# Kernel optimization log

Measured on AMD Instinct MI355X. Metric: run time of the kernel, lower is better.

## Reference

```python
import jax, jax.numpy as jnp
import numpy as np

NUM_GROUPS = 32
EPS = 1e-6


def group_norm(x, gamma, beta):
    # x: [B, C, H, W]; GroupNorm over (channels-in-group, H, W)
    B, C, H, W = x.shape
    xg = x.reshape(B, NUM_GROUPS, C // NUM_GROUPS, H, W)
    mean = xg.mean(axis=(2, 3, 4), keepdims=True)
    var = xg.var(axis=(2, 3, 4), keepdims=True)
    xn = ((xg - mean) * jax.lax.rsqrt(var + EPS)).reshape(B, C, H, W)
    return xn * gamma[None, :, None, None] + beta[None, :, None, None]


def conv1x1(x, w, b):
    # 1x1 conv == channel-mixing matmul. w: [C_out, C_in]
    return jnp.einsum('bchw,oc->bohw', x, w) + b[None, :, None, None]


def setup_inputs() -> dict:
    key = jax.random.key(0)
    ks = jax.random.split(key, 6)
    B, C, H, W = 8, 256, 64, 64
    s = 1.0 / np.sqrt(C)  # fan-in scaled weights (like Conv2d default)
    inp = {
        'x': jax.random.normal(ks[0], (B, C, H, W), jnp.float32),
        'gamma': jnp.ones((C,), jnp.float32),
        'beta': jnp.zeros((C,), jnp.float32),
        'wq': jax.random.normal(ks[1], (C, C), jnp.float32) * s,
        'bq': jnp.zeros((C,), jnp.float32),
        'wk': jax.random.normal(ks[2], (C, C), jnp.float32) * s,
        'bk': jnp.zeros((C,), jnp.float32),
        'wv': jax.random.normal(ks[3], (C, C), jnp.float32) * s,
        'bv': jnp.zeros((C,), jnp.float32),
        'wo': jax.random.normal(ks[4], (C, C), jnp.float32) * s,
        'bo': jnp.zeros((C,), jnp.float32),
    }
    return inp


def reference(x, gamma, beta, wq, bq, wk, bk, wv, bv, wo, bo):
    B, C, H, W = x.shape
    h = group_norm(x, gamma, beta)
    q = conv1x1(h, wq, bq)
    k = conv1x1(h, wk, bk)
    v = conv1x1(h, wv, bv)
    # elu + 1 feature map (nonnegative kernel features)
    q = jax.nn.elu(q) + 1.0
    k = jax.nn.elu(k) + 1.0
    N = H * W
    kf = k.reshape(B, C, N)            # [B, C, N]
    vf = v.reshape(B, C, N)            # [B, C, N]
    qf = q.reshape(B, C, N)            # [B, C, N]
    # kv = k @ v^T : [B, C, C]
    kv = jnp.einsum('bcn,bdn->bcd', kf, vf)
    # h_out[b, n, d] = sum_c q[b, c, n] * kv[b, c, d]; stored channel-first
    h_out = jnp.einsum('bcn,bcd->bdn', qf, kv).reshape(B, C, H, W)
    return x + conv1x1(h_out, wo, bo)
```

## Files before the change

### kernel.cpp

```cpp
#include <hip/hip_runtime.h>
#include <math.h>

#define C_DIM 256
#define N_DIM 4096
#define B_DIM 8

typedef __attribute__((ext_vector_type(8))) short bf16x8;
typedef __attribute__((ext_vector_type(4))) float f32x4;
typedef __attribute__((ext_vector_type(8))) unsigned short us8;
typedef __attribute__((ext_vector_type(4))) unsigned short us4;

__device__ inline unsigned short f2bf(float f) {
    unsigned int u = __float_as_uint(f);
    u += 0x7fffu + ((u >> 16) & 1u);
    return (unsigned short)(u >> 16);
}

__device__ inline void gload_lds16(const void* g, void* l) {
    __builtin_amdgcn_global_load_lds(
        (const __attribute__((address_space(1))) unsigned int*)g,
        (__attribute__((address_space(3))) unsigned int*)l, 16, 0, 0);
}

__global__ __launch_bounds__(256) void prep_kernel(
    const float* __restrict__ wq, const float* __restrict__ wk,
    const float* __restrict__ wv, const float* __restrict__ wo,
    const float* __restrict__ bk, const float* __restrict__ bv,
    const float* __restrict__ x,
    unsigned short* __restrict__ wqb, unsigned short* __restrict__ wkvb,
    unsigned short* __restrict__ wob, float* __restrict__ bkv,
    float2* __restrict__ sums)
{
    int z = blockIdx.x;
    int t = threadIdx.x;
    if (z < 256) {
        const float* s; unsigned short* d;
        int which = z >> 6;
        if (which == 0)      { s = wq; d = wqb; }
        else if (which == 1) { s = wk; d = wkvb; }
        else if (which == 2) { s = wv; d = wkvb + 65536; }
        else                 { s = wo; d = wob; }
        int idx = (z & 63) * 1024 + t * 4;
        float4 v = *(const float4*)(s + idx);
        us4 r; r[0] = f2bf(v.x); r[1] = f2bf(v.y); r[2] = f2bf(v.z); r[3] = f2bf(v.w);
        *(us4*)(d + idx) = r;
    } else if (z == 256) {
        bkv[t]       = bk[t];
        bkv[t + 256] = bv[t];
    } else {
        int bc = z - 257;
        const float* xc = x + (size_t)bc * N_DIM;
        float s = 0.f, q = 0.f;
        for (int i = t; i < 1024; i += 256) {
            float4 v = ((const float4*)xc)[i];
            s += v.x + v.y + v.z + v.w;
            q += v.x*v.x + v.y*v.y + v.z*v.z + v.w*v.w;
        }
        #pragma unroll
        for (int off = 32; off > 0; off >>= 1) {
            s += __shfl_down(s, off);
            q += __shfl_down(q, off);
        }
        __shared__ float red[8];
        int w = t >> 6;
        if ((t & 63) == 0) { red[w*2] = s; red[w*2+1] = q; }
        __syncthreads();
        if (t == 0) {
            sums[bc] = make_float2(red[0]+red[2]+red[4]+red[6],
                                   red[1]+red[3]+red[5]+red[7]);
        }
    }
}

__global__ __launch_bounds__(256) void gn_apply(const float* __restrict__ x,
                                                const float2* __restrict__ sums,
                                                const float* __restrict__ gamma,
                                                const float* __restrict__ beta,
                                                unsigned short* __restrict__ hT) {
    int b = blockIdx.y, n0 = blockIdx.x * 64;
    int t = threadIdx.x;
    __shared__ float scale[256], shift[256];
    __shared__ unsigned short trans[64][264];

    {
        int c = t;
        int gbase = c & ~7;
        float s = 0.f, q = 0.f;
        #pragma unroll
        for (int j = 0; j < 8; j++) {
            float2 u = sums[b*256 + gbase + j];
            s += u.x; q += u.y;
        }
        float mean = s * (1.f/32768.f);
        float var  = q * (1.f/32768.f) - mean*mean;
        float inv  = rsqrtf(var + 1e-6f);
        float gm = gamma[c] * inv;
        scale[c] = gm;
        shift[c] = beta[c] - mean * gm;
    }
    __syncthreads();

    #pragma unroll
    for (int it = 0; it < 16; it++) {
        int c  = it*16 + (t >> 4);
        int nl = (t & 15) * 4;
        float4 v = *(const float4*)(x + ((size_t)(b*C_DIM + c))*N_DIM + n0 + nl);
        float sc = scale[c], sh = shift[c];
        trans[nl+0][c] = f2bf(v.x*sc + sh);
        trans[nl+1][c] = f2bf(v.y*sc + sh);
        trans[nl+2][c] = f2bf(v.z*sc + sh);
        trans[nl+3][c] = f2bf(v.w*sc + sh);
    }
    __syncthreads();

    #pragma unroll
    for (int it = 0; it < 8; it++) {
        int nl = it*8 + (t >> 5);
        int cb = (t & 31) * 8;
        us8 vv = *(us8*)&trans[nl][cb];
        *(us8*)(hT + ((size_t)b*N_DIM + n0 + nl)*C_DIM + cb) = vv;
    }
}

__global__ __launch_bounds__(256) void kvred(const float* __restrict__ src, unsigned short* __restrict__ dst) {
    int gi = (blockIdx.x * 256 + threadIdx.x) * 4;
    int b = gi >> 16, idx = gi & 65535;
    float4 a = make_float4(0.f,0.f,0.f,0.f);
    #pragma unroll
    for (int sp = 0; sp < 16; sp++) {
        float4 v = *(const float4*)(src + (((size_t)b*16 + sp) << 16) + idx);
        a.x += v.x; a.y += v.y; a.z += v.z; a.w += v.w;
    }
    us4 r; r[0] = f2bf(a.x); r[1] = f2bf(a.y); r[2] = f2bf(a.z); r[3] = f2bf(a.w);
    *(us4*)(dst + ((size_t)b << 16) + idx) = r;
}

template<int MODE>
__device__ __forceinline__ void gemm_body(
    const unsigned short* __restrict__ Ab, const unsigned short* __restrict__ Bb,
    const float* __restrict__ bias, const float* __restrict__ residb,
    void* __restrict__ Cb,
    int N, int K, int k0, int Ks, int m_blk, int n_blk, bool elu,
    char* smem)
{
    unsigned short* lds = (unsigned short*)smem;

    int t = threadIdx.x;
    int w = t >> 6, l = t & 63;
    int wm = w >> 1, wn = w & 1;
    int l15 = l & 15, quad = l >> 4;

    int srow = w * 16 + (l >> 2);
    int skc  = (((l & 3) ^ ((l >> 3) & 3)) * 8);

    f32x4 acc[4][4];
    #pragma unroll
    for (int i = 0; i < 4; i++)
        #pragma unroll
        for (int j = 0; j < 4; j++)
            #pragma unroll
            for (int r = 0; r < 4; r++) acc[i][j][r] = 0.f;

    auto stage = [&](int buf, int kt) {
        unsigned short* Asl = lds + buf*8192 + t*8;
        unsigned short* Bsl = Asl + 4096;
        #pragma unroll
        for (int rep = 0; rep < 2; rep++) {
            gload_lds16(Ab + (size_t)(m_blk + rep*64 + srow) * K + kt + skc, Asl + rep*2048);
            gload_lds16(Bb + (size_t)(n_blk + rep*64 + srow) * K + kt + skc, Bsl + rep*2048);
        }
    };

    const int nt = Ks >> 5;

    stage(0, k0);
    if (nt > 1) stage(1, k0 + 32);

    int rsw = (l15 >> 1) & 3;
    int acol = (quad ^ rsw) * 8;

    int bufc = 0;
    for (int kt = 0; kt < nt; ++kt) {
        if (kt + 1 < nt) asm volatile("s_waitcnt vmcnt(4)" ::: "memory");
        else             asm volatile("s_waitcnt vmcnt(0)" ::: "memory");
        __builtin_amdgcn_s_barrier();
        __builtin_amdgcn_sched_barrier(0);
        if (kt + 2 < nt) {
            int bufn = bufc + 2; if (bufn >= 3) bufn -= 3;
            stage(bufn, k0 + (kt + 2) * 32);
        }
        __builtin_amdgcn_sched_barrier(0);

        const unsigned short* Aw = lds + bufc*8192 + (wm*64 + l15)*32 + acol;
        const unsigned short* Bw = lds + bufc*8192 + 4096 + (wn*64 + l15)*32 + acol;
        bf16x8 af[4], bfr[4];
        #pragma unroll
        for (int i = 0; i < 4; i++) af[i]  = *(const bf16x8*)(Aw + i*512);
        #pragma unroll
        for (int j = 0; j < 4; j++) bfr[j] = *(const bf16x8*)(Bw + j*512);
        __builtin_amdgcn_s_setprio(1);
        #pragma unroll
        for (int i = 0; i < 4; i++)
            #pragma unroll
            for (int j = 0; j < 4; j++)
                acc[i][j] = __builtin_amdgcn_mfma_f32_16x16x32_bf16(af[i], bfr[j], acc[i][j], 0, 0, 0);
        __builtin_amdgcn_s_setprio(0);
        bufc = (bufc == 2) ? 0 : bufc + 1;
    }
    __syncthreads();

    if (MODE == 0 || MODE == 1 || MODE == 4) {
        unsigned short* ep = (unsigned short*)smem;
        unsigned short* Cp = (unsigned short*)Cb;
        #pragma unroll
        for (int h = 0; h < 2; h++) {
            if (wm == h) {
                int row0 = quad*4;
                int col0 = wn*64 + l15;
                #pragma unroll
                for (int i = 0; i < 4; i++) {
                    #pragma unroll
                    for (int j = 0; j < 4; j++) {
                        int cl = col0 + j*16;
                        #pragma unroll
                        for (int r = 0; r < 4; r++) {
                            int rl = row0 + i*16 + r;
                            float val = acc[i][j][r];
                            if (MODE == 0) {
                                val += bias[n_blk + cl];
                                val = val > 0.f ? val + 1.f : __expf(val);
                            } else if (MODE == 1) {
                                val += bias[m_blk + h*64 + rl];
                                if (elu) val = val > 0.f ? val + 1.f : __expf(val);
                            }
                            ep[rl*136 + cl] = f2bf(val);
                        }
                    }
                }
            }
            __syncthreads();
            #pragma unroll
            for (int it = 0; it < 4; it++) {
                int row = it*16 + (t >> 4);
                int col = (t & 15) * 8;
                us8 vv = *(us8*)(ep + row*136 + col);
                *(us8*)(Cp + (size_t)(m_blk + h*64 + row) * N + n_blk + col) = vv;
            }
            __syncthreads();
        }
    } else {
        float* ep32 = (float*)smem;
        float* Cp = (float*)Cb;
        #pragma unroll
        for (int h = 0; h < 2; h++) {
            if (wm == h) {
                int row0 = quad*4;
                int col0 = wn*64 + l15;
                #pragma unroll
                for (int i = 0; i < 4; i++)
                    #pragma unroll
                    for (int j = 0; j < 4; j++)
                        #pragma unroll
                        for (int r = 0; r < 4; r++)
                            ep32[(row0 + i*16 + r)*140 + col0 + j*16] = acc[i][j][r];
            }
            __syncthreads();
            #pragma unroll
            for (int it = 0; it < 8; it++) {
                int rl  = it*8 + (t >> 5);
                int row = m_blk + h*64 + rl;
                int col = (t & 31) * 4;
                f32x4 vv = *(f32x4*)(ep32 + rl*140 + col);
                if (MODE == 5) {
                    float bi = bias[row];
                    float4 rv = *(const float4*)(residb + (size_t)row * N + n_blk + col);
                    vv[0] += bi + rv.x; vv[1] += bi + rv.y;
                    vv[2] += bi + rv.z; vv[3] += bi + rv.w;
                }
                *(f32x4*)(Cp + (size_t)row * N + n_blk + col) = vv;
            }
            __syncthreads();
        }
    }
}

__global__ __launch_bounds__(256) void qkv_kernel(
    const unsigned short* __restrict__ hT, const unsigned short* __restrict__ wqb,
    const unsigned short* __restrict__ wkvb,
    const float* __restrict__ bq, const float* __restrict__ bkv,
    unsigned short* __restrict__ qT, unsigned short* __restrict__ kvbuf)
{
    __shared__ __align__(16) char smem[49152];
    int z = blockIdx.x;
    if (z < 512) {
        int b = z >> 6, rem = z & 63;
        int m_blk = (rem >> 1) * 128, n_blk = (rem & 1) * 128;
        gemm_body<0>(hT + (size_t)b*1048576, wqb, bq, nullptr,
                     qT + (size_t)b*1048576,
                     256, 256, 0, 256, m_blk, n_blk, true, smem);
    } else {
        int iz = z - 512;
        int b = iz >> 7, rem = iz & 127;
        int m_blk = (rem >> 5) * 128, n_blk = (rem & 31) * 128;
        gemm_body<1>(wkvb, hT + (size_t)b*1048576, bkv, nullptr,
                     kvbuf + (size_t)b*2097152,
                     4096, 256, 0, 256, m_blk, n_blk, m_blk < 256, smem);
    }
}

template<int MODE>
__global__ __launch_bounds__(256) void gemm_nt(
    const unsigned short* __restrict__ A, const unsigned short* __restrict__ B,
    const float* __restrict__ bias, const float* __restrict__ resid,
    void* __restrict__ Cout,
    int N, int K, int splits,
    size_t sA, size_t sB, size_t sC, size_t sR, int elem4)
{
    __shared__ __align__(16) char smem[49152];
    int b  = blockIdx.z / splits;
    int sp = blockIdx.z % splits;
    int Ks = K / splits;
    size_t cbase = (MODE == 3) ? ((size_t)(b*splits + sp)) * sC : (size_t)b * sC;
    void* Cb = elem4 ? (void*)((float*)Cout + cbase) : (void*)((unsigned short*)Cout + cbase);
    gemm_body<MODE>(A + b*sA, B + b*sB, bias,
                    resid ? resid + b*sR : nullptr, Cb,
                    N, K, sp*Ks, Ks, blockIdx.y*128, blockIdx.x*128, false, smem);
}

extern "C" void kernel_launch(void* const* d_in, const int* in_sizes, int n_in,
                              void* d_out, int out_size, void* d_ws, size_t ws_size,
                              hipStream_t stream) {
    const float* x     = (const float*)d_in[0];
    const float* gamma = (const float*)d_in[1];
    const float* beta  = (const float*)d_in[2];
    const float* wq    = (const float*)d_in[3];
    const float* bq    = (const float*)d_in[4];
    const float* wk    = (const float*)d_in[5];
    const float* bk    = (const float*)d_in[6];
    const float* wv    = (const float*)d_in[7];
    const float* bv    = (const float*)d_in[8];
    const float* wo    = (const float*)d_in[9];
    const float* bo    = (const float*)d_in[10];
    float* out = (float*)d_out;

    const size_t TEN = (size_t)B_DIM * C_DIM * N_DIM;
    unsigned short* ws16  = (unsigned short*)d_ws;
    unsigned short* hT    = ws16;
    unsigned short* qT    = hT    + TEN;
    unsigned short* kvbuf = qT    + TEN;
    unsigned short* kvb   = kvbuf + 2*TEN;
    unsigned short* M2b   = kvb   + 524288;
    unsigned short* wqb   = M2b   + 524288;
    unsigned short* wkvb  = wqb   + 65536;
    unsigned short* wob   = wkvb  + 131072;
    float*          bkv   = (float*)(wob + 65536);
    float2*         sums  = (float2*)(bkv + 512);
    float*          kvf   = (float*)(sums + 2048);

    prep_kernel<<<dim3(2305), 256, 0, stream>>>(wq, wk, wv, wo, bk, bv, x,
                                                wqb, wkvb, wob, bkv, sums);
    gn_apply<<<dim3(N_DIM/64, B_DIM), 256, 0, stream>>>(x, sums, gamma, beta, hT);
    qkv_kernel<<<dim3(1536), 256, 0, stream>>>(hT, wqb, wkvb, bq, bkv, qT, kvbuf);
    gemm_nt<3><<<dim3(2, 2, B_DIM*16), 256, 0, stream>>>(
        kvbuf, kvbuf + 1048576, nullptr, nullptr, kvf,
        256, 4096, 16, 2097152, 2097152, 65536, 0, 1);
    kvred<<<dim3(512), 256, 0, stream>>>(kvf, kvb);
    gemm_nt<4><<<dim3(2, 2, B_DIM), 256, 0, stream>>>(
        wob, kvb, nullptr, nullptr, M2b,
        256, 256, 1, 0, 65536, 65536, 0, 0);
    gemm_nt<5><<<dim3(32, 2, B_DIM), 256, 0, stream>>>(
        M2b, qT, bo, x, out,
        4096, 256, 1, 65536, 1048576, 1048576, 1048576, 1);
}
```

Baseline: 188.7 us.

## Replace QKV projection GEMM with weight-stationary kernel streaming activations from global

The QKV projection moves to a new kernel that loads a whole 128x256 weight slab into LDS once, pre-swizzled by the prep kernel to avoid bank conflicts. Activation rows are read straight from global memory into registers with a three-deep software prefetch, in place of the generic double-buffered LDS GEMM. Outputs are written directly from registers with bias and ELU applied, dropping the LDS epilogue staging. The cost is heavier register use, uncoalesced scattered stores for q (2-byte writes), and 64 KB of LDS per block, which may lower occupancy.

```diff
diff --git a/kernel.cpp b/kernel.cpp
--- a/kernel.cpp
+++ b/kernel.cpp
@@ -27,23 +27,30 @@
     const float* __restrict__ wv, const float* __restrict__ wo,
     const float* __restrict__ bk, const float* __restrict__ bv,
     const float* __restrict__ x,
-    unsigned short* __restrict__ wqb, unsigned short* __restrict__ wkvb,
-    unsigned short* __restrict__ wob, float* __restrict__ bkv,
-    float2* __restrict__ sums)
+    unsigned short* __restrict__ wqs, unsigned short* __restrict__ wks,
+    unsigned short* __restrict__ wvs, unsigned short* __restrict__ wob,
+    float* __restrict__ bkv, float2* __restrict__ sums)
 {
     int z = blockIdx.x;
     int t = threadIdx.x;
     if (z < 256) {
-        const float* s; unsigned short* d;
         int which = z >> 6;
-        if (which == 0)      { s = wq; d = wqb; }
-        else if (which == 1) { s = wk; d = wkvb; }
-        else if (which == 2) { s = wv; d = wkvb + 65536; }
-        else                 { s = wo; d = wob; }
+        const float* s = which == 0 ? wq : which == 1 ? wk : which == 2 ? wv : wo;
+        unsigned short* d = which == 0 ? wqs : which == 1 ? wks : which == 2 ? wvs : wob;
         int idx = (z & 63) * 1024 + t * 4;
         float4 v = *(const float4*)(s + idx);
         us4 r; r[0] = f2bf(v.x); r[1] = f2bf(v.y); r[2] = f2bf(v.z); r[3] = f2bf(v.w);
-        *(us4*)(d + idx) = r;
+        int dst;
+        if (which == 3) {
+            dst = idx;
+        } else {
+            int o = idx >> 8, k = idx & 255;
+            int ch = o >> 7, ol = o & 127;
+            int c  = k >> 3;
+            int cs = (c & ~7) | ((c ^ o) & 7);
+            dst = ch * 32768 + ol * 256 + cs * 8 + (k & 7);
+        }
+        *(us4*)(d + dst) = r;
     } else if (z == 256) {
         bkv[t]       = bk[t];
         bkv[t + 256] = bv[t];
@@ -135,6 +142,117 @@
     *(us4*)(dst + ((size_t)b << 16) + idx) = r;
 }
 
+__global__ __launch_bounds__(256) void qkv_ws(
+    const unsigned short* __restrict__ hT,
+    const unsigned short* __restrict__ wqs, const unsigned short* __restrict__ wks,
+    const unsigned short* __restrict__ wvs,
+    const float* __restrict__ bq, const float* __restrict__ bkv,
+    unsigned short* __restrict__ qT, unsigned short* __restrict__ kvbuf)
+{
+    __shared__ __align__(16) unsigned short W[32768];
+    int z = blockIdx.x;
+    int role    = z >> 9;
+    int chunk   = (z >> 1) & 255;
+    int ch      = z & 1;
+    int rowbase = chunk * 128;
+    int colbase = ch * 128;
+    int t = threadIdx.x;
+
+    const unsigned short* wsrc = (role == 0 ? wqs : role == 1 ? wks : wvs) + ch * 32768;
+
+    #pragma unroll
+    for (int it = 0; it < 16; ++it)
+        gload_lds16(wsrc + (it*256 + t)*8, W + (it*256 + t)*8);
+
+    int w = t >> 6, l = t & 63;
+    int wr = w >> 1, wc = w & 1;
+    int l15 = l & 15, quad = l >> 4;
+    int x7 = l15 & 7;
+
+    const float* bsrc = role == 0 ? bq : bkv + (role == 2 ? 256 : 0);
+    float bias[4];
+    #pragma unroll
+    for (int j = 0; j < 4; ++j) bias[j] = bsrc[colbase + wc*64 + j*16 + l15];
+
+    const unsigned short* aB[4];
+    #pragma unroll
+    for (int i = 0; i < 4; ++i)
+        aB[i] = hT + (size_t)(rowbase + wr*64 + i*16 + l15) * 256 + quad*8;
+
+    asm volatile("s_waitcnt vmcnt(0)" ::: "memory");
+    __syncthreads();
+
+    bf16x8 A[3][4];
+    #pragma unroll
+    for (int i = 0; i < 4; ++i) A[0][i] = *(const bf16x8*)(aB[i]);
+    #pragma unroll
+    for (int i = 0; i < 4; ++i) A[1][i] = *(const bf16x8*)(aB[i] + 32);
+
+    f32x4 acc[4][4];
+    #pragma unroll
+    for (int i = 0; i < 4; ++i)
+        #pragma unroll
+        for (int j = 0; j < 4; ++j)
+            #pragma unroll
+            for (int r = 0; r < 4; ++r) acc[i][j][r] = 0.f;
+
+    #pragma unroll
+    for (int s = 0; s < 8; ++s) {
+        int coff = ((s >> 1)*8 + ((quad + 4*(s & 1)) ^ x7)) * 8;
+        bf16x8 bfr[4];
+        #pragma unroll
+        for (int j = 0; j < 4; ++j)
+            bfr[j] = *(const bf16x8*)(W + (wc*64 + j*16 + l15)*256 + coff);
+        if (s + 2 < 8) {
+            #pragma unroll
+            for (int i = 0; i < 4; ++i)
+                A[(s + 2) % 3][i] = *(const bf16x8*)(aB[i] + (s + 2)*32);
+        }
+        #pragma unroll
+        for (int i = 0; i < 4; ++i)
+            #pragma unroll
+            for (int j = 0; j < 4; ++j)
+                acc[i][j] = __builtin_amdgcn_mfma_f32_16x16x32_bf16(A[s % 3][i], bfr[j], acc[i][j], 0, 0, 0);
+    }
+
+    if (role == 0) {
+        #pragma unroll
+        for (int i = 0; i < 4; ++i) {
+            int g = rowbase + wr*64 + i*16 + quad*4;
+            #pragma unroll
+            for (int j = 0; j < 4; ++j) {
+                int col = colbase + wc*64 + j*16 + l15;
+                #pragma unroll
+                for (int r = 0; r < 4; ++r) {
+                    float v = acc[i][j][r] + bias[j];
+                    v = v > 0.f ? v + 1.f : __expf(v);
+                    qT[(size_t)(g + r)*256 + col] = f2bf(v);
+                }
+            }
+        }
+    } else {
+        int b = rowbase >> 12, n0 = rowbase & 4095;
+        int ccb = (role == 2) ? 256 : 0;
+        unsigned short* base = kvbuf + (size_t)b * 2097152;
+        #pragma unroll
+        for (int i = 0; i < 4; ++i) {
+            int n = n0 + wr*64 + i*16 + quad*4;
+            #pragma unroll
+            for (int j = 0; j < 4; ++j) {
+                int cc = ccb + colbase + wc*64 + j*16 + l15;
+                us4 pk;
+                #pragma unroll
+                for (int r = 0; r < 4; ++r) {
+                    float v = acc[i][j][r] + bias[j];
+                    if (role == 1) v = v > 0.f ? v + 1.f : __expf(v);
+                    pk[r] = f2bf(v);
+                }
+                *(us4*)(base + (size_t)cc*4096 + n) = pk;
+            }
+        }
+    }
+}
+
 template<int MODE>
 __device__ __forceinline__ void gemm_body(
     const unsigned short* __restrict__ Ab, const unsigned short* __restrict__ Bb,
@@ -209,7 +327,7 @@
     }
     __syncthreads();
 
-    if (MODE == 0 || MODE == 1 || MODE == 4) {
+    if (MODE == 4) {
         unsigned short* ep = (unsigned short*)smem;
         unsigned short* Cp = (unsigned short*)Cb;
         #pragma unroll
@@ -225,15 +343,7 @@
                         #pragma unroll
                         for (int r = 0; r < 4; r++) {
                             int rl = row0 + i*16 + r;
-                            float val = acc[i][j][r];
-                            if (MODE == 0) {
-                                val += bias[n_blk + cl];
-                                val = val > 0.f ? val + 1.f : __expf(val);
-                            } else if (MODE == 1) {
-                                val += bias[m_blk + h*64 + rl];
-                                if (elu) val = val > 0.f ? val + 1.f : __expf(val);
-                            }
-                            ep[rl*136 + cl] = f2bf(val);
+                            ep[rl*136 + cl] = f2bf(acc[i][j][r]);
                         }
                     }
                 }
@@ -281,30 +391,6 @@
             }
             __syncthreads();
         }
-    }
-}
-
-__global__ __launch_bounds__(256) void qkv_kernel(
-    const unsigned short* __restrict__ hT, const unsigned short* __restrict__ wqb,
-    const unsigned short* __restrict__ wkvb,
-    const float* __restrict__ bq, const float* __restrict__ bkv,
-    unsigned short* __restrict__ qT, unsigned short* __restrict__ kvbuf)
-{
-    __shared__ __align__(16) char smem[49152];
-    int z = blockIdx.x;
-    if (z < 512) {
-        int b = z >> 6, rem = z & 63;
-        int m_blk = (rem >> 1) * 128, n_blk = (rem & 1) * 128;
-        gemm_body<0>(hT + (size_t)b*1048576, wqb, bq, nullptr,
-                     qT + (size_t)b*1048576,
-                     256, 256, 0, 256, m_blk, n_blk, true, smem);
-    } else {
-        int iz = z - 512;
-        int b = iz >> 7, rem = iz & 127;
-        int m_blk = (rem >> 5) * 128, n_blk = (rem & 31) * 128;
-        gemm_body<1>(wkvb, hT + (size_t)b*1048576, bkv, nullptr,
-                     kvbuf + (size_t)b*2097152,
-                     4096, 256, 0, 256, m_blk, n_blk, m_blk < 256, smem);
     }
 }
 
@@ -350,17 +436,18 @@
     unsigned short* kvbuf = qT    + TEN;
     unsigned short* kvb   = kvbuf + 2*TEN;
     unsigned short* M2b   = kvb   + 524288;
-    unsigned short* wqb   = M2b   + 524288;
-    unsigned short* wkvb  = wqb   + 65536;
-    unsigned short* wob   = wkvb  + 131072;
+    unsigned short* wqs   = M2b   + 524288;
+    unsigned short* wks   = wqs   + 65536;
+    unsigned short* wvs   = wks   + 65536;
+    unsigned short* wob   = wvs   + 65536;
     float*          bkv   = (float*)(wob + 65536);
     float2*         sums  = (float2*)(bkv + 512);
     float*          kvf   = (float*)(sums + 2048);
 
     prep_kernel<<<dim3(2305), 256, 0, stream>>>(wq, wk, wv, wo, bk, bv, x,
-                                                wqb, wkvb, wob, bkv, sums);
+                                                wqs, wks, wvs, wob, bkv, sums);
     gn_apply<<<dim3(N_DIM/64, B_DIM), 256, 0, stream>>>(x, sums, gamma, beta, hT);
-    qkv_kernel<<<dim3(1536), 256, 0, stream>>>(hT, wqb, wkvb, bq, bkv, qT, kvbuf);
+    qkv_ws<<<dim3(1536), 256, 0, stream>>>(hT, wqs, wks, wvs, bq, bkv, qT, kvbuf);
     gemm_nt<3><<<dim3(2, 2, B_DIM*16), 256, 0, stream>>>(
         kvbuf, kvbuf + 1048576, nullptr, nullptr, kvf,
         256, 4096, 16, 2097152, 2097152, 65536, 0, 1);
```

Result: no change. 192.1 us (+1.8%).
